# Kernel tuning notes

Measured on AMD Instinct MI355X. Metric: run time of the kernel, lower is better.

## Reference

```python
import jax, jax.numpy as jnp
import numpy as np

# ---- module hyperparameters (init_kwargs) ----
FRAME_PERIOD = 120
SAMPLE_RATE = 24000
FFT_LENGTH = 2048
DEFAULT_F0 = 500.0
Q1 = -0.15
F_MIN = 3.0 * SAMPLE_RATE / (FFT_LENGTH - 3)
EPS_SAFE = 1e-12                      # safeguard noise inside windowing (WORLD kMySafeGuardMinimum)
EPS_F32 = float(np.finfo(np.float32).eps)  # torch.finfo(x.dtype).eps
TAU = 2.0 * np.pi
MAX_F0_STATIC = 600.0                 # static bound on f0 for the smoothing mirror pad
K_PAD = int(MAX_F0_STATIC * 2.0 / 3.0 * FFT_LENGTH / SAMPLE_RATE) + 2

B, T = 8, 120000
N_FRAMES = T // FRAME_PERIOD + 1      # 1001


def setup_inputs() -> dict:
    key = jax.random.key(0)
    kx, kf = jax.random.split(key)
    x = jax.random.normal(kx, (B, T), dtype=jnp.float32)
    # realistic voiced f0 in [100, 400] Hz (always > F_MIN)
    f0 = 100.0 + 300.0 * jax.random.uniform(kf, (B, N_FRAMES), dtype=jnp.float32)
    return {"x": x, "f0": f0}


def _interp_last(c, pos):
    # linear interpolation of c (..., M) at float positions pos (..., K) (interp1Q)
    M = c.shape[-1]
    lo = jnp.clip(jnp.floor(pos).astype(jnp.int32), 0, M - 2)
    frac = pos - lo.astype(pos.dtype)
    c_lo = jnp.take_along_axis(c, lo, axis=-1)
    c_hi = jnp.take_along_axis(c, lo + 1, axis=-1)
    return c_lo + (c_hi - c_lo) * frac


def reference(x, f0):
    L = FFT_LENGTH
    half = L // 2
    K1 = half + 1
    fs = SAMPLE_RATE

    f0 = jnp.where(f0 <= F_MIN, DEFAULT_F0, f0)[..., None]          # (B,N,1)
    f0 = jax.lax.stop_gradient(f0)                                   # .detach() in torch

    # ---- pitch-synchronous Hanning windowing (get_windowed_waveform, ratio=3, bias=0) ----
    n = jnp.arange(f0.shape[1])
    rel = jnp.arange(L) - half                                       # sample offset from frame center
    idx = jnp.clip(n[:, None] * FRAME_PERIOD + rel[None, :], 0, x.shape[-1] - 1)  # (N,L) safe_index
    frames = x[:, idx]                                               # (B,N,L)
    hwl = jnp.round(1.5 * fs / f0)                                   # half window length (B,N,1)
    mask = (jnp.abs(rel) <= hwl).astype(x.dtype)                     # (B,N,L)
    win = (0.5 * jnp.cos(jnp.pi * rel / (1.5 * fs) * f0) + 0.5) * mask
    win = win / jnp.sqrt(jnp.sum(win * win, -1, keepdims=True))      # normalize_power=True
    noise = jax.random.normal(jax.random.key(42), frames.shape, frames.dtype)
    wav = frames * win + EPS_SAFE * noise * mask
    wav = wav - win * (jnp.sum(wav, -1, keepdims=True) / jnp.sum(win, -1, keepdims=True))

    # ---- power spectrum (Spectrum, out_format='power', eps=0) ----
    P = jnp.abs(jnp.fft.rfft(wav, n=L, axis=-1)) ** 2                # (B,N,K1)

    # ---- DC correction: mirror the spectrum around f0 for bins below f0 ----
    k = jnp.arange(K1)
    rate = f0 * L / fs                                               # f0 in bins (B,N,1)
    m = rate - k                                                     # mirror position (B,N,K1)
    lo = jnp.clip(jnp.floor(m).astype(jnp.int32), 0, K1 - 2)
    frac = m - lo.astype(m.dtype)
    repl = jnp.take_along_axis(P, lo, -1) * (1 - frac) + jnp.take_along_axis(P, lo + 1, -1) * frac
    P = P + jnp.where(k < 1 + jnp.floor(rate), repl, 0.0)

    # ---- linear (rectangular) smoothing of width 2/3*f0 Hz via mirrored cumsum ----
    width = f0 * (2.0 / 3.0)                                         # Hz (B,N,1)
    j = jnp.arange(K1 + 2 * K_PAD) - K_PAD
    refl = jnp.abs(j)
    refl = jnp.where(refl > half, L - refl, refl)                    # even reflection at 0 and L/2
    C = jnp.cumsum(P[..., refl] * (fs / L), -1)                      # cumulative integral (B,N,K1+2K)
    wbins = width * L / fs
    pos_lo = k - 0.5 * wbins + (K_PAD - 0.5)                         # grid origin -(K-0.5)*fs/L
    P = (_interp_last(C, pos_lo + wbins) - _interp_last(C, pos_lo)) / width

    # ---- safeguard noise (power_spectrum += |randn| * finfo.eps) ----
    P = P + jnp.abs(jax.random.normal(jax.random.key(43), P.shape, P.dtype)) * EPS_F32

    # ---- cepstral liftering ----
    quef = k / fs                                                    # quefrency axis (K1,)
    z = f0 * quef                                                    # (B,N,K1)
    sl = jnp.sinc(z).at[..., 0].set(1.0)                             # smoothing lifter
    cl = 1 - 2 * Q1 + 2 * Q1 * jnp.cos(TAU * z)                      # compensation lifter
    cep = jnp.fft.irfft(jnp.log(P), n=L, axis=-1)[..., :K1]
    log_power_spectrum = jnp.fft.hfft(cep * sl * cl, axis=-1)[..., :K1]
    return log_power_spectrum
```

## Files before the change

### kernel.cpp

```cpp
#include <hip/hip_runtime.h>
#include <math.h>

#define NFFT   2048
#define N1     1024
#define K1     1025
#define KPAD   36
#define MTOT   1097
#define NFRAMES 1001
#define TLEN   120000
#define BATCH  8
#define FPER   120
#define PIF 3.14159265358979323846f

#define A(i) ((i) + ((i) >> 4))

typedef float2 cpx;
__device__ __forceinline__ cpx cmul(cpx a, cpx b) {
    return make_float2(a.x * b.x - a.y * b.y, a.x * b.y + a.y * b.x);
}
__device__ __forceinline__ cpx cadd(cpx a, cpx b) { return make_float2(a.x + b.x, a.y + b.y); }
__device__ __forceinline__ cpx csub(cpx a, cpx b) { return make_float2(a.x - b.x, a.y - b.y); }

__device__ __forceinline__ int brev10(int v) {
    return (int)(__brev((unsigned)v) >> 22);
}

template<int H>
__device__ __forceinline__ void dif_fused(cpx* c, int tid, cpx w1) {
    int r  = tid & (H / 2 - 1);
    int i0 = (tid / (H / 2)) * (2 * H) + r;
    int ia = A(i0), ib = A(i0 + H / 2), ic = A(i0 + H), id = A(i0 + 3 * H / 2);
    cpx a = c[ia], b = c[ib], cc = c[ic], d = c[id];
    cpx w1n = make_float2(w1.y, -w1.x);
    cpx w2  = make_float2(w1.x * w1.x - w1.y * w1.y, 2.0f * w1.x * w1.y);
    cpx a1 = cadd(a, cc);
    cpx c1 = cmul(csub(a, cc), w1);
    cpx b1 = cadd(b, d);
    cpx d1 = cmul(csub(b, d), w1n);
    c[ia] = cadd(a1, b1);
    c[ib] = cmul(csub(a1, b1), w2);
    c[ic] = cadd(c1, d1);
    c[id] = cmul(csub(c1, d1), w2);
    __syncthreads();
}

__device__ __forceinline__ void dif_last2(cpx* c, int tid) {
    int i0 = 4 * tid;
    int ia = A(i0), ib = A(i0 + 1), ic = A(i0 + 2), id = A(i0 + 3);
    cpx a = c[ia], b = c[ib], cc = c[ic], d = c[id];
    cpx a1 = cadd(a, cc);
    cpx c1 = csub(a, cc);
    cpx b1 = cadd(b, d);
    cpx bd = csub(b, d);
    cpx d1 = make_float2(bd.y, -bd.x);
    c[ia] = cadd(a1, b1);
    c[ib] = csub(a1, b1);
    c[ic] = cadd(c1, d1);
    c[id] = csub(c1, d1);
    __syncthreads();
}

__device__ __forceinline__ void fft1024(cpx* c, int tid, const cpx* tw) {
    dif_fused<512>(c, tid, tw[0]);
    dif_fused<128>(c, tid, tw[1]);
    dif_fused<32>(c, tid, tw[2]);
    dif_fused<8>(c, tid, tw[3]);
    dif_last2(c, tid);
}

__device__ __forceinline__ cpx unpack_k(const cpx* s_c, int k, cpx w) {
    int kk = k & (N1 - 1);
    int mm = (N1 - kk) & (N1 - 1);
    cpx Zk = s_c[A(brev10(kk))];
    cpx Zm = s_c[A(brev10(mm))];
    float Ex = 0.5f * (Zk.x + Zm.x), Ey = 0.5f * (Zk.y - Zm.y);
    float Ox = 0.5f * (Zk.y + Zm.y), Oy = 0.5f * (Zm.x - Zk.x);
    return make_float2(Ex + w.x * Ox - w.y * Oy,
                       Ey + w.x * Oy + w.y * Ox);
}

__global__ __launch_bounds__(256)
void cheaptrick_kernel(const float* __restrict__ x,
                       const float* __restrict__ f0in,
                       float* __restrict__ out) {
    __shared__ cpx   s_c[1088];
    __shared__ float s_P[1026];
    __shared__ float s_C[MTOT];
    __shared__ float s_scan[16];

    const int tid  = threadIdx.x;
    const int lane = tid & 63;
    const int wid  = tid >> 6;
    const int n    = blockIdx.x;
    const int b    = blockIdx.y;

    float f0 = f0in[b * NFRAMES + n];
    const float F_MIN = 72000.0f / 2045.0f;
    if (f0 <= F_MIN) f0 = 500.0f;

    float fr[8], wn[8];
    float hwl = rintf(36000.0f / f0);
    float s_w2 = 0.0f, s_w = 0.0f, s_fw = 0.0f;
    int base_idx = n * FPER - N1 + 8 * tid;
#pragma unroll
    for (int j = 0; j < 8; ++j) {
        int l = 8 * tid + j;
        float relf = (float)(l - N1);
        int idx = max(0, min(TLEN - 1, base_idx + j));
        fr[j] = x[b * TLEN + idx];
        float w = 0.0f;
        if (fabsf(relf) <= hwl) {
            w = 0.5f * __cosf(PIF * relf / 36000.0f * f0) + 0.5f;
        }
        wn[j] = w;
        s_w2 += w * w;
        s_w  += w;
        s_fw += fr[j] * w;
    }
#pragma unroll
    for (int off = 32; off > 0; off >>= 1) {
        s_w2 += __shfl_down(s_w2, off, 64);
        s_w  += __shfl_down(s_w,  off, 64);
        s_fw += __shfl_down(s_fw, off, 64);
    }
    if (lane == 0) {
        s_scan[wid]     = s_w2;
        s_scan[4 + wid] = s_w;
        s_scan[8 + wid] = s_fw;
    }
    __syncthreads();
    float w2sum = s_scan[0] + s_scan[1] + s_scan[2] + s_scan[3];
    float wsum  = s_scan[4] + s_scan[5] + s_scan[6] + s_scan[7];
    float fwsum = s_scan[8] + s_scan[9] + s_scan[10] + s_scan[11];
    float wscale = 1.0f / sqrtf(w2sum);
    float dc = fwsum / wsum;
    __syncthreads();

#pragma unroll
    for (int j = 0; j < 4; ++j) {
        float v0 = wscale * wn[2 * j]     * (fr[2 * j]     - dc);
        float v1 = wscale * wn[2 * j + 1] * (fr[2 * j + 1] - dc);
        s_c[A(4 * tid + j)] = make_float2(v0, v1);
    }

    cpx tw[4], u2048;
    {
        float sn, cs;
        __sincosf(-PIF * (float)(tid & 255) * (1.0f / 512.0f), &sn, &cs);
        tw[0] = make_float2(cs, sn);
        __sincosf(-PIF * (float)(tid & 63) * (1.0f / 128.0f), &sn, &cs);
        tw[1] = make_float2(cs, sn);
        __sincosf(-PIF * (float)(tid & 15) * (1.0f / 32.0f), &sn, &cs);
        tw[2] = make_float2(cs, sn);
        __sincosf(-PIF * (float)(tid & 3) * (1.0f / 8.0f), &sn, &cs);
        tw[3] = make_float2(cs, sn);
        __sincosf(-PIF * (float)tid * (1.0f / 1024.0f), &sn, &cs);
        u2048 = make_float2(cs, sn);
    }
    const float RH = 0.70710678118654752f;
    const cpx W8[5] = { make_float2(1.0f, 0.0f), make_float2(RH, -RH),
                        make_float2(0.0f, -1.0f), make_float2(-RH, -RH),
                        make_float2(-1.0f, 0.0f) };

    __syncthreads();
    fft1024(s_c, tid, tw);

#pragma unroll
    for (int c5 = 0; c5 < 5; ++c5) {
        int k = tid + (c5 << 8);
        if (k < K1) {
            cpx X = unpack_k(s_c, k, cmul(u2048, W8[c5]));
            s_P[k] = X.x * X.x + X.y * X.y;
        }
    }
    __syncthreads();

    float rate = f0 * (2048.0f / 24000.0f);
    int kmax = (int)floorf(rate);
    float repl = 0.0f;
    if (tid <= kmax) {
        float m = rate - (float)tid;
        int lo = (int)floorf(m);
        lo = max(0, min(K1 - 2, lo));
        float frac = m - (float)lo;
        repl = s_P[lo] * (1.0f - frac) + s_P[lo + 1] * frac;
    }
    __syncthreads();
    if (tid <= kmax) s_P[tid] += repl;
    __syncthreads();

    float loc[5];
    float run = 0.0f;
    int basej = tid * 5;
#pragma unroll
    for (int c = 0; c < 5; ++c) {
        int j = basej + c;
        float v = 0.0f;
        if (j < MTOT) {
            int a = abs(j - KPAD);
            if (a > N1) a = NFFT - a;
            v = s_P[a] * (24000.0f / 2048.0f);
        }
        run += v;
        loc[c] = run;
    }
    float v = run;
#pragma unroll
    for (int off = 1; off < 64; off <<= 1) {
        float o = __shfl_up(v, off, 64);
        if (lane >= off) v += o;
    }
    if (lane == 63) s_scan[wid] = v;
    __syncthreads();
    float wbase = 0.0f;
#pragma unroll
    for (int w = 0; w < 4; ++w) wbase += (w < wid) ? s_scan[w] : 0.0f;
    float prefix = wbase + v - run;
#pragma unroll
    for (int c = 0; c < 5; ++c) {
        int j = basej + c;
        if (j < MTOT) s_C[j] = prefix + loc[c];
    }
    __syncthreads();

    float width = f0 * (2.0f / 3.0f);
    float wbins = width * (2048.0f / 24000.0f);
#pragma unroll
    for (int c5 = 0; c5 < 5; ++c5) {
        int k = tid + (c5 << 8);
        if (k < K1) {
            float pos_lo = (float)k - 0.5f * wbins + ((float)KPAD - 0.5f);
            float pos_hi = pos_lo + wbins;
            int llo = (int)floorf(pos_lo); llo = max(0, min(MTOT - 2, llo));
            float flo = pos_lo - (float)llo;
            float clo = s_C[llo] + (s_C[llo + 1] - s_C[llo]) * flo;
            int lhi = (int)floorf(pos_hi); lhi = max(0, min(MTOT - 2, lhi));
            float fhi = pos_hi - (float)lhi;
            float chi = s_C[lhi] + (s_C[lhi + 1] - s_C[lhi]) * fhi;
            s_P[k] = __logf((chi - clo) / width);
        }
    }
    __syncthreads();

#pragma unroll
    for (int c = 0; c < 4; ++c) {
        int m = tid + (c << 8);
        int j0 = 2 * m;
        int j1 = 2 * m + 1;
        float v0 = (j0 <= N1) ? s_P[j0] : s_P[NFFT - j0];
        float v1 = (j1 <= N1) ? s_P[j1] : s_P[NFFT - j1];
        s_c[A(m)] = make_float2(v0, v1);
    }
    __syncthreads();
    fft1024(s_c, tid, tw);

#pragma unroll
    for (int c5 = 0; c5 < 5; ++c5) {
        int k = tid + (c5 << 8);
        if (k < K1) {
            cpx X = unpack_k(s_c, k, cmul(u2048, W8[c5]));
            float cep = X.x * (1.0f / 2048.0f);
            float pz = PIF * f0 * ((float)k * (1.0f / 24000.0f));
            float s = __sinf(pz);
            float sl = (k != 0) ? (s / pz) : 1.0f;
            float cl = 1.0f + 0.6f * s * s;
            s_P[k] = cep * sl * cl;
        }
    }
    __syncthreads();

#pragma unroll
    for (int c = 0; c < 4; ++c) {
        int m = tid + (c << 8);
        int j0 = 2 * m;
        int j1 = 2 * m + 1;
        float v0 = (j0 <= N1) ? s_P[j0] : s_P[NFFT - j0];
        float v1 = (j1 <= N1) ? s_P[j1] : s_P[NFFT - j1];
        s_c[A(m)] = make_float2(v0, v1);
    }
    __syncthreads();
    fft1024(s_c, tid, tw);

    float* orow = out + (size_t)(b * NFRAMES + n) * K1;
#pragma unroll
    for (int c5 = 0; c5 < 5; ++c5) {
        int k = tid + (c5 << 8);
        if (k < K1) {
            cpx X = unpack_k(s_c, k, cmul(u2048, W8[c5]));
            orow[k] = X.x;
        }
    }
}

extern "C" void kernel_launch(void* const* d_in, const int* in_sizes, int n_in,
                              void* d_out, int out_size, void* d_ws, size_t ws_size,
                              hipStream_t stream) {
    (void)in_sizes; (void)n_in; (void)d_ws; (void)ws_size; (void)out_size;
    const float* x  = (const float*)d_in[0];
    const float* f0 = (const float*)d_in[1];
    float* out = (float*)d_out;
    dim3 grid(NFRAMES, BATCH);
    hipLaunchKernelGGL(cheaptrick_kernel, grid, dim3(256), 0, stream, x, f0, out);
}
```

Measured before the change: 161.5 us.

## Process two frames per block, interleaving their FFTs to halve barriers

Each block now handles two adjacent frames. The two frames' FFT butterflies and per-stage work are interleaved, so every __syncthreads is shared by both and each thread has more independent work (ILP) between barriers. s_C is aliased onto the complex FFT buffers to limit LDS growth. The cost is more registers and LDS per block and half as many blocks, which may lower occupancy and leave a tail at the odd final frame.

```diff
diff --git a/kernel.cpp b/kernel.cpp
--- a/kernel.cpp
+++ b/kernel.cpp
@@ -26,46 +26,73 @@
 }
 
 template<int H>
-__device__ __forceinline__ void dif_fused(cpx* c, int tid, cpx w1) {
+__device__ __forceinline__ void dif_stage2(cpx* cA, cpx* cB, int tid, cpx w1) {
     int r  = tid & (H / 2 - 1);
     int i0 = (tid / (H / 2)) * (2 * H) + r;
     int ia = A(i0), ib = A(i0 + H / 2), ic = A(i0 + H), id = A(i0 + 3 * H / 2);
-    cpx a = c[ia], b = c[ib], cc = c[ic], d = c[id];
     cpx w1n = make_float2(w1.y, -w1.x);
     cpx w2  = make_float2(w1.x * w1.x - w1.y * w1.y, 2.0f * w1.x * w1.y);
-    cpx a1 = cadd(a, cc);
-    cpx c1 = cmul(csub(a, cc), w1);
-    cpx b1 = cadd(b, d);
-    cpx d1 = cmul(csub(b, d), w1n);
-    c[ia] = cadd(a1, b1);
-    c[ib] = cmul(csub(a1, b1), w2);
-    c[ic] = cadd(c1, d1);
-    c[id] = cmul(csub(c1, d1), w2);
-    __syncthreads();
-}
-
-__device__ __forceinline__ void dif_last2(cpx* c, int tid) {
+    cpx aA = cA[ia], bA = cA[ib], ccA = cA[ic], dA = cA[id];
+    cpx aB = cB[ia], bB = cB[ib], ccB = cB[ic], dB = cB[id];
+    {
+        cpx a1 = cadd(aA, ccA);
+        cpx c1 = cmul(csub(aA, ccA), w1);
+        cpx b1 = cadd(bA, dA);
+        cpx d1 = cmul(csub(bA, dA), w1n);
+        cA[ia] = cadd(a1, b1);
+        cA[ib] = cmul(csub(a1, b1), w2);
+        cA[ic] = cadd(c1, d1);
+        cA[id] = cmul(csub(c1, d1), w2);
+    }
+    {
+        cpx a1 = cadd(aB, ccB);
+        cpx c1 = cmul(csub(aB, ccB), w1);
+        cpx b1 = cadd(bB, dB);
+        cpx d1 = cmul(csub(bB, dB), w1n);
+        cB[ia] = cadd(a1, b1);
+        cB[ib] = cmul(csub(a1, b1), w2);
+        cB[ic] = cadd(c1, d1);
+        cB[id] = cmul(csub(c1, d1), w2);
+    }
+    __syncthreads();
+}
+
+__device__ __forceinline__ void dif_last2_2(cpx* cA, cpx* cB, int tid) {
     int i0 = 4 * tid;
     int ia = A(i0), ib = A(i0 + 1), ic = A(i0 + 2), id = A(i0 + 3);
-    cpx a = c[ia], b = c[ib], cc = c[ic], d = c[id];
-    cpx a1 = cadd(a, cc);
-    cpx c1 = csub(a, cc);
-    cpx b1 = cadd(b, d);
-    cpx bd = csub(b, d);
-    cpx d1 = make_float2(bd.y, -bd.x);
-    c[ia] = cadd(a1, b1);
-    c[ib] = csub(a1, b1);
-    c[ic] = cadd(c1, d1);
-    c[id] = csub(c1, d1);
-    __syncthreads();
-}
-
-__device__ __forceinline__ void fft1024(cpx* c, int tid, const cpx* tw) {
-    dif_fused<512>(c, tid, tw[0]);
-    dif_fused<128>(c, tid, tw[1]);
-    dif_fused<32>(c, tid, tw[2]);
-    dif_fused<8>(c, tid, tw[3]);
-    dif_last2(c, tid);
+    {
+        cpx a = cA[ia], b = cA[ib], cc = cA[ic], d = cA[id];
+        cpx a1 = cadd(a, cc);
+        cpx c1 = csub(a, cc);
+        cpx b1 = cadd(b, d);
+        cpx bd = csub(b, d);
+        cpx d1 = make_float2(bd.y, -bd.x);
+        cA[ia] = cadd(a1, b1);
+        cA[ib] = csub(a1, b1);
+        cA[ic] = cadd(c1, d1);
+        cA[id] = csub(c1, d1);
+    }
+    {
+        cpx a = cB[ia], b = cB[ib], cc = cB[ic], d = cB[id];
+        cpx a1 = cadd(a, cc);
+        cpx c1 = csub(a, cc);
+        cpx b1 = cadd(b, d);
+        cpx bd = csub(b, d);
+        cpx d1 = make_float2(bd.y, -bd.x);
+        cB[ia] = cadd(a1, b1);
+        cB[ib] = csub(a1, b1);
+        cB[ic] = cadd(c1, d1);
+        cB[id] = csub(c1, d1);
+    }
+    __syncthreads();
+}
+
+__device__ __forceinline__ void fft1024_2(cpx* cA, cpx* cB, int tid, const cpx* tw) {
+    dif_stage2<512>(cA, cB, tid, tw[0]);
+    dif_stage2<128>(cA, cB, tid, tw[1]);
+    dif_stage2<32>(cA, cB, tid, tw[2]);
+    dif_stage2<8>(cA, cB, tid, tw[3]);
+    dif_last2_2(cA, cB, tid);
 }
 
 __device__ __forceinline__ cpx unpack_k(const cpx* s_c, int k, cpx w) {
@@ -79,69 +106,83 @@
                        Ey + w.x * Oy + w.y * Ox);
 }
 
+__device__ __forceinline__ void extract_pack(const float* __restrict__ xrow,
+                                             int n, float f0, cpx* s_c,
+                                             volatile float* scanseg,
+                                             int tid, int lane, int wid) {
+    float fr[8], wn[8];
+    float hwl = rintf(36000.0f / f0);
+    float s_w2 = 0.0f, s_w = 0.0f, s_fw = 0.0f;
+    int base_idx = n * FPER - N1 + 8 * tid;
+#pragma unroll
+    for (int j = 0; j < 8; ++j) {
+        int l = 8 * tid + j;
+        float relf = (float)(l - N1);
+        int idx = max(0, min(TLEN - 1, base_idx + j));
+        fr[j] = xrow[idx];
+        float w = 0.0f;
+        if (fabsf(relf) <= hwl) {
+            w = 0.5f * __cosf(PIF * relf / 36000.0f * f0) + 0.5f;
+        }
+        wn[j] = w;
+        s_w2 += w * w;
+        s_w  += w;
+        s_fw += fr[j] * w;
+    }
+#pragma unroll
+    for (int off = 32; off > 0; off >>= 1) {
+        s_w2 += __shfl_down(s_w2, off, 64);
+        s_w  += __shfl_down(s_w,  off, 64);
+        s_fw += __shfl_down(s_fw, off, 64);
+    }
+    if (lane == 0) {
+        scanseg[wid]     = s_w2;
+        scanseg[4 + wid] = s_w;
+        scanseg[8 + wid] = s_fw;
+    }
+    __syncthreads();
+    float w2sum = scanseg[0] + scanseg[1] + scanseg[2] + scanseg[3];
+    float wsum  = scanseg[4] + scanseg[5] + scanseg[6] + scanseg[7];
+    float fwsum = scanseg[8] + scanseg[9] + scanseg[10] + scanseg[11];
+    float wscale = 1.0f / sqrtf(w2sum);
+    float dc = fwsum / wsum;
+#pragma unroll
+    for (int j = 0; j < 4; ++j) {
+        float v0 = wscale * wn[2 * j]     * (fr[2 * j]     - dc);
+        float v1 = wscale * wn[2 * j + 1] * (fr[2 * j + 1] - dc);
+        s_c[A(4 * tid + j)] = make_float2(v0, v1);
+    }
+}
+
 __global__ __launch_bounds__(256)
 void cheaptrick_kernel(const float* __restrict__ x,
                        const float* __restrict__ f0in,
                        float* __restrict__ out) {
-    __shared__ cpx   s_c[1088];
-    __shared__ float s_P[1026];
-    __shared__ float s_C[MTOT];
-    __shared__ float s_scan[16];
+    __shared__ cpx   s_cA[1088];
+    __shared__ cpx   s_cB[1088];
+    __shared__ float s_PA[1026];
+    __shared__ float s_PB[1026];
+    __shared__ float s_scan[32];
+    float* s_CA = (float*)s_cA;
+    float* s_CB = (float*)s_cB;
 
     const int tid  = threadIdx.x;
     const int lane = tid & 63;
     const int wid  = tid >> 6;
-    const int n    = blockIdx.x;
     const int b    = blockIdx.y;
-
-    float f0 = f0in[b * NFRAMES + n];
+    const int nA   = 2 * blockIdx.x;
+    const bool hasB = (nA + 1) < NFRAMES;
+    const int nB   = hasB ? (nA + 1) : nA;
+
     const float F_MIN = 72000.0f / 2045.0f;
-    if (f0 <= F_MIN) f0 = 500.0f;
-
-    float fr[8], wn[8];
-    float hwl = rintf(36000.0f / f0);
-    float s_w2 = 0.0f, s_w = 0.0f, s_fw = 0.0f;
-    int base_idx = n * FPER - N1 + 8 * tid;
-#pragma unroll
-    for (int j = 0; j < 8; ++j) {
-        int l = 8 * tid + j;
-        float relf = (float)(l - N1);
-        int idx = max(0, min(TLEN - 1, base_idx + j));
-        fr[j] = x[b * TLEN + idx];
-        float w = 0.0f;
-        if (fabsf(relf) <= hwl) {
-            w = 0.5f * __cosf(PIF * relf / 36000.0f * f0) + 0.5f;
-        }
-        wn[j] = w;
-        s_w2 += w * w;
-        s_w  += w;
-        s_fw += fr[j] * w;
-    }
-#pragma unroll
-    for (int off = 32; off > 0; off >>= 1) {
-        s_w2 += __shfl_down(s_w2, off, 64);
-        s_w  += __shfl_down(s_w,  off, 64);
-        s_fw += __shfl_down(s_fw, off, 64);
-    }
-    if (lane == 0) {
-        s_scan[wid]     = s_w2;
-        s_scan[4 + wid] = s_w;
-        s_scan[8 + wid] = s_fw;
-    }
-    __syncthreads();
-    float w2sum = s_scan[0] + s_scan[1] + s_scan[2] + s_scan[3];
-    float wsum  = s_scan[4] + s_scan[5] + s_scan[6] + s_scan[7];
-    float fwsum = s_scan[8] + s_scan[9] + s_scan[10] + s_scan[11];
-    float wscale = 1.0f / sqrtf(w2sum);
-    float dc = fwsum / wsum;
-    __syncthreads();
-
-#pragma unroll
-    for (int j = 0; j < 4; ++j) {
-        float v0 = wscale * wn[2 * j]     * (fr[2 * j]     - dc);
-        float v1 = wscale * wn[2 * j + 1] * (fr[2 * j + 1] - dc);
-        s_c[A(4 * tid + j)] = make_float2(v0, v1);
-    }
+    float f0A = f0in[b * NFRAMES + nA];
+    if (f0A <= F_MIN) f0A = 500.0f;
+    float f0B = f0in[b * NFRAMES + nB];
+    if (f0B <= F_MIN) f0B = 500.0f;
+
+    const float* xrow = x + (size_t)b * TLEN;
+    extract_pack(xrow, nA, f0A, s_cA, s_scan,      tid, lane, wid);
+    extract_pack(xrow, nB, f0B, s_cB, s_scan + 16, tid, lane, wid);
 
     cpx tw[4], u2048;
     {
@@ -163,81 +204,112 @@
                         make_float2(-1.0f, 0.0f) };
 
     __syncthreads();
-    fft1024(s_c, tid, tw);
+    fft1024_2(s_cA, s_cB, tid, tw);
 
 #pragma unroll
     for (int c5 = 0; c5 < 5; ++c5) {
         int k = tid + (c5 << 8);
         if (k < K1) {
-            cpx X = unpack_k(s_c, k, cmul(u2048, W8[c5]));
-            s_P[k] = X.x * X.x + X.y * X.y;
-        }
-    }
-    __syncthreads();
-
-    float rate = f0 * (2048.0f / 24000.0f);
-    int kmax = (int)floorf(rate);
-    float repl = 0.0f;
-    if (tid <= kmax) {
-        float m = rate - (float)tid;
+            cpx w = cmul(u2048, W8[c5]);
+            cpx XA = unpack_k(s_cA, k, w);
+            s_PA[k] = XA.x * XA.x + XA.y * XA.y;
+            cpx XB = unpack_k(s_cB, k, w);
+            s_PB[k] = XB.x * XB.x + XB.y * XB.y;
+        }
+    }
+    __syncthreads();
+
+    float rateA = f0A * (2048.0f / 24000.0f);
+    float rateB = f0B * (2048.0f / 24000.0f);
+    int kmaxA = (int)floorf(rateA);
+    int kmaxB = (int)floorf(rateB);
+    float replA = 0.0f, replB = 0.0f;
+    if (tid <= kmaxA) {
+        float m = rateA - (float)tid;
         int lo = (int)floorf(m);
         lo = max(0, min(K1 - 2, lo));
         float frac = m - (float)lo;
-        repl = s_P[lo] * (1.0f - frac) + s_P[lo + 1] * frac;
-    }
-    __syncthreads();
-    if (tid <= kmax) s_P[tid] += repl;
-    __syncthreads();
-
-    float loc[5];
-    float run = 0.0f;
+        replA = s_PA[lo] * (1.0f - frac) + s_PA[lo + 1] * frac;
+    }
+    if (tid <= kmaxB) {
+        float m = rateB - (float)tid;
+        int lo = (int)floorf(m);
+        lo = max(0, min(K1 - 2, lo));
+        float frac = m - (float)lo;
+        replB = s_PB[lo] * (1.0f - frac) + s_PB[lo + 1] * frac;
+    }
+    __syncthreads();
+    if (tid <= kmaxA) s_PA[tid] += replA;
+    if (tid <= kmaxB) s_PB[tid] += replB;
+    __syncthreads();
+
+    float locA[5], locB[5];
+    float runA = 0.0f, runB = 0.0f;
     int basej = tid * 5;
 #pragma unroll
     for (int c = 0; c < 5; ++c) {
         int j = basej + c;
-        float v = 0.0f;
+        float vA = 0.0f, vB = 0.0f;
         if (j < MTOT) {
             int a = abs(j - KPAD);
             if (a > N1) a = NFFT - a;
-            v = s_P[a] * (24000.0f / 2048.0f);
-        }
-        run += v;
-        loc[c] = run;
-    }
-    float v = run;
+            vA = s_PA[a] * (24000.0f / 2048.0f);
+            vB = s_PB[a] * (24000.0f / 2048.0f);
+        }
+        runA += vA; locA[c] = runA;
+        runB += vB; locB[c] = runB;
+    }
+    float vA = runA, vB = runB;
 #pragma unroll
     for (int off = 1; off < 64; off <<= 1) {
-        float o = __shfl_up(v, off, 64);
-        if (lane >= off) v += o;
-    }
-    if (lane == 63) s_scan[wid] = v;
-    __syncthreads();
-    float wbase = 0.0f;
-#pragma unroll
-    for (int w = 0; w < 4; ++w) wbase += (w < wid) ? s_scan[w] : 0.0f;
-    float prefix = wbase + v - run;
+        float oA = __shfl_up(vA, off, 64);
+        float oB = __shfl_up(vB, off, 64);
+        if (lane >= off) { vA += oA; vB += oB; }
+    }
+    if (lane == 63) { s_scan[wid] = vA; s_scan[16 + wid] = vB; }
+    __syncthreads();
+    float wbA = 0.0f, wbB = 0.0f;
+#pragma unroll
+    for (int w = 0; w < 4; ++w) {
+        if (w < wid) { wbA += s_scan[w]; wbB += s_scan[16 + w]; }
+    }
+    float prefA = wbA + vA - runA;
+    float prefB = wbB + vB - runB;
 #pragma unroll
     for (int c = 0; c < 5; ++c) {
         int j = basej + c;
-        if (j < MTOT) s_C[j] = prefix + loc[c];
-    }
-    __syncthreads();
-
-    float width = f0 * (2.0f / 3.0f);
-    float wbins = width * (2048.0f / 24000.0f);
+        if (j < MTOT) { s_CA[j] = prefA + locA[c]; s_CB[j] = prefB + locB[c]; }
+    }
+    __syncthreads();
+
+    float widthA = f0A * (2.0f / 3.0f), wbinsA = widthA * (2048.0f / 24000.0f);
+    float widthB = f0B * (2.0f / 3.0f), wbinsB = widthB * (2048.0f / 24000.0f);
 #pragma unroll
     for (int c5 = 0; c5 < 5; ++c5) {
         int k = tid + (c5 << 8);
         if (k < K1) {
-            float pos_lo = (float)k - 0.5f * wbins + ((float)KPAD - 0.5f);
-            float pos_hi = pos_lo + wbins;
-            int llo = (int)floorf(pos_lo); llo = max(0, min(MTOT - 2, llo));
-            float flo = pos_lo - (float)llo;
-            float clo = s_C[llo] + (s_C[llo + 1] - s_C[llo]) * flo;
-            int lhi = (int)floorf(pos_hi); lhi = max(0, min(MTOT - 2, lhi));
-            float fhi = pos_hi - (float)lhi;
-            float chi = s_C[lhi] + (s_C[lhi + 1] - s_C[lhi]) * fhi;
-            s_P[k] = __logf((chi - clo) / width);
+            {
+                float pos_lo = (float)k - 0.5f * wbinsA + ((float)KPAD - 0.5f);
+                float pos_hi = pos_lo + wbinsA;
+                int llo = (int)floorf(pos_lo); llo = max(0, min(MTOT - 2, llo));
+                float flo = pos_lo - (float)llo;
+                float clo = s_CA[llo] + (s_CA[llo + 1] - s_CA[llo]) * flo;
+                int lhi = (int)floorf(pos_hi); lhi = max(0, min(MTOT - 2, lhi));
+                float fhi = pos_hi - (float)lhi;
+                float chi = s_CA[lhi] + (s_CA[lhi + 1] - s_CA[lhi]) * fhi;
+                s_PA[k] = __logf((chi - clo) / widthA);
+            }
+            {
+                float pos_lo = (float)k - 0.5f * wbinsB + ((float)KPAD - 0.5f);
+                float pos_hi = pos_lo + wbinsB;
+                int llo = (int)floorf(pos_lo); llo = max(0, min(MTOT - 2, llo));
+                float flo = pos_lo - (float)llo;
+                float clo = s_CB[llo] + (s_CB[llo + 1] - s_CB[llo]) * flo;
+                int lhi = (int)floorf(pos_hi); lhi = max(0, min(MTOT - 2, lhi));
+                float fhi = pos_hi - (float)lhi;
+                float chi = s_CB[lhi] + (s_CB[lhi + 1] - s_CB[lhi]) * fhi;
+                s_PB[k] = __logf((chi - clo) / widthB);
+            }
         }
     }
     __syncthreads();
@@ -247,24 +319,39 @@
         int m = tid + (c << 8);
         int j0 = 2 * m;
         int j1 = 2 * m + 1;
-        float v0 = (j0 <= N1) ? s_P[j0] : s_P[NFFT - j0];
-        float v1 = (j1 <= N1) ? s_P[j1] : s_P[NFFT - j1];
-        s_c[A(m)] = make_float2(v0, v1);
-    }
-    __syncthreads();
-    fft1024(s_c, tid, tw);
+        float a0 = (j0 <= N1) ? s_PA[j0] : s_PA[NFFT - j0];
+        float a1 = (j1 <= N1) ? s_PA[j1] : s_PA[NFFT - j1];
+        s_cA[A(m)] = make_float2(a0, a1);
+        float b0 = (j0 <= N1) ? s_PB[j0] : s_PB[NFFT - j0];
+        float b1 = (j1 <= N1) ? s_PB[j1] : s_PB[NFFT - j1];
+        s_cB[A(m)] = make_float2(b0, b1);
+    }
+    __syncthreads();
+    fft1024_2(s_cA, s_cB, tid, tw);
 
 #pragma unroll
     for (int c5 = 0; c5 < 5; ++c5) {
         int k = tid + (c5 << 8);
         if (k < K1) {
-            cpx X = unpack_k(s_c, k, cmul(u2048, W8[c5]));
-            float cep = X.x * (1.0f / 2048.0f);
-            float pz = PIF * f0 * ((float)k * (1.0f / 24000.0f));
-            float s = __sinf(pz);
-            float sl = (k != 0) ? (s / pz) : 1.0f;
-            float cl = 1.0f + 0.6f * s * s;
-            s_P[k] = cep * sl * cl;
+            cpx w = cmul(u2048, W8[c5]);
+            {
+                cpx X = unpack_k(s_cA, k, w);
+                float cep = X.x * (1.0f / 2048.0f);
+                float pz = PIF * f0A * ((float)k * (1.0f / 24000.0f));
+                float s = __sinf(pz);
+                float sl = (k != 0) ? (s / pz) : 1.0f;
+                float cl = 1.0f + 0.6f * s * s;
+                s_PA[k] = cep * sl * cl;
+            }
+            {
+                cpx X = unpack_k(s_cB, k, w);
+                float cep = X.x * (1.0f / 2048.0f);
+                float pz = PIF * f0B * ((float)k * (1.0f / 24000.0f));
+                float s = __sinf(pz);
+                float sl = (k != 0) ? (s / pz) : 1.0f;
+                float cl = 1.0f + 0.6f * s * s;
+                s_PB[k] = cep * sl * cl;
+            }
         }
     }
     __syncthreads();
@@ -274,20 +361,29 @@
         int m = tid + (c << 8);
         int j0 = 2 * m;
         int j1 = 2 * m + 1;
-        float v0 = (j0 <= N1) ? s_P[j0] : s_P[NFFT - j0];
-        float v1 = (j1 <= N1) ? s_P[j1] : s_P[NFFT - j1];
-        s_c[A(m)] = make_float2(v0, v1);
-    }
-    __syncthreads();
-    fft1024(s_c, tid, tw);
-
-    float* orow = out + (size_t)(b * NFRAMES + n) * K1;
+        float a0 = (j0 <= N1) ? s_PA[j0] : s_PA[NFFT - j0];
+        float a1 = (j1 <= N1) ? s_PA[j1] : s_PA[NFFT - j1];
+        s_cA[A(m)] = make_float2(a0, a1);
+        float b0 = (j0 <= N1) ? s_PB[j0] : s_PB[NFFT - j0];
+        float b1 = (j1 <= N1) ? s_PB[j1] : s_PB[NFFT - j1];
+        s_cB[A(m)] = make_float2(b0, b1);
+    }
+    __syncthreads();
+    fft1024_2(s_cA, s_cB, tid, tw);
+
+    float* orowA = out + (size_t)(b * NFRAMES + nA) * K1;
+    float* orowB = out + (size_t)(b * NFRAMES + nB) * K1;
 #pragma unroll
     for (int c5 = 0; c5 < 5; ++c5) {
         int k = tid + (c5 << 8);
         if (k < K1) {
-            cpx X = unpack_k(s_c, k, cmul(u2048, W8[c5]));
-            orow[k] = X.x;
+            cpx w = cmul(u2048, W8[c5]);
+            cpx XA = unpack_k(s_cA, k, w);
+            orowA[k] = XA.x;
+            if (hasB) {
+                cpx XB = unpack_k(s_cB, k, w);
+                orowB[k] = XB.x;
+            }
         }
     }
 }
@@ -299,6 +395,6 @@
     const float* x  = (const float*)d_in[0];
     const float* f0 = (const float*)d_in[1];
     float* out = (float*)d_out;
-    dim3 grid(NFRAMES, BATCH);
+    dim3 grid((NFRAMES + 1) / 2, BATCH);
     hipLaunchKernelGGL(cheaptrick_kernel, grid, dim3(256), 0, stream, x, f0, out);
 }
```

After: 166.9 us. 1.03x slower.
